# Optimization experiments

Hardware: AMD Instinct MI355X
Metric: run time of the kernel (lower is better)

The kernel has to match this reference:

```python
import jax, jax.numpy as jnp
import numpy as np

B, L, DIN, DH, DE = 16, 128, 768, 300, 100
ALPHA = 0.2
NEG = -9e15


def setup_inputs() -> dict:
    key = jax.random.key(0)
    k = jax.random.split(key, 7)
    s = lambda fan: 1.0 / np.sqrt(fan)
    return {
        "x": jax.random.normal(k[0], (B, L, DIN), jnp.float32),
        "adj": jax.random.randint(k[1], (B, L, L), 0, 2, jnp.int32),
        "edge_embedding": jax.random.normal(k[2], (B, L, L, DE), jnp.float32),
        "W": jax.random.normal(k[3], (DIN, DH), jnp.float32) * s(DIN),
        "a": jax.random.normal(k[4], (2 * DH, 1), jnp.float32) * s(2 * DH),
        "edge_map_w": jax.random.normal(k[5], (DH, DE), jnp.float32) * s(DE),
        "edge_map_b": jnp.zeros((DH,), jnp.float32),
        "edge_lin_w": jax.random.normal(k[6], (1, DH), jnp.float32) * s(DH),
        "edge_lin_b": jnp.zeros((1,), jnp.float32),
    }


def _forward(x, edge_embedding, W, a, edge_map_w, edge_map_b, edge_lin_w, edge_lin_b, adj):
    h = x @ W  # [B, L, DH]
    # Faithful to torch: h.repeat_interleave(L, dim=2).view(B, L*L, DH) scrambles
    # features: a_input_first[b, i*L+j, d] = h[b, i, (j*DH + d) // L].
    # So e1[b,i,j] = sum_d h[b,i,(j*DH+d)//L] * a[d] = h[b,i] . V[j], with V[j,k] =
    # sum of a[d] over d where (j*DH+d)//L == k. Build V once by scatter-add.
    idx = (jnp.arange(L)[:, None] * DH + jnp.arange(DH)[None, :]) // L  # [L, DH], values in [0, DH)
    a_first = a[:DH, 0]
    V = jnp.zeros((L, DH), h.dtype).at[jnp.arange(L)[:, None], idx].add(a_first[None, :])  # [L, DH]
    e1 = jnp.einsum('bik,jk->bij', h, V)  # [B, L, L]
    # Second half: h.repeat_interleave(L, dim=0).view(...) gives plain h_j tiling.
    e2 = h @ a[DH:, 0]  # [B, L], broadcast over i
    e = jax.nn.leaky_relu(e1 + e2[:, None, :], ALPHA)  # [B, L, L]
    # Edge-weight gate (use_edge_weight == 'yes'); note torch relu result is discarded.
    em = edge_embedding @ edge_map_w.T + edge_map_b  # [B, L, L, DH]
    ew = jax.nn.sigmoid(em @ edge_lin_w.T + edge_lin_b)[..., 0]  # [B, L, L]
    e_final = e * ew
    att = jax.nn.softmax(jnp.where(adj > 0, e_final, NEG), axis=2)  # dropout off (eval)
    return h + jnp.matmul(att, h)  # residual add, concat=False


def reference(x, adj, edge_embedding, W, a, edge_map_w, edge_map_b, edge_lin_w, edge_lin_b):
    return _forward(x, edge_embedding, W, a, edge_map_w, edge_map_b, edge_lin_w, edge_lin_b, adj)
```

## Files before the change

### kernel.cpp

```cpp
#include <hip/hip_runtime.h>
#include <hip/hip_bf16.h>


#define L 128
#define DH 300
#define DIN 768
#define DE 100
#define SPLITK 4
#define MROWS 2048
#define SL ((size_t)MROWS * DH)

typedef __bf16 bf16x8 __attribute__((ext_vector_type(8)));
typedef float f32x4 __attribute__((ext_vector_type(4)));
typedef unsigned short ushort_t;

__device__ __forceinline__ ushort_t f2bf(float f) {
    __bf16 h = (__bf16)f;
    ushort_t u;
    __builtin_memcpy(&u, &h, 2);
    return u;
}

__global__ __launch_bounds__(256) void k_small(
    const float* __restrict__ A,
    const float* __restrict__ EMW,
    const float* __restrict__ EMB,
    const float* __restrict__ ELW,
    const float* __restrict__ ELB,
    float* __restrict__ CV, float* __restrict__ C0,
    float* __restrict__ VW, int* __restrict__ VCOL)
{
    int t = threadIdx.x;
    if (blockIdx.x == 0) {
        if (t < DE) {
            float s = 0.f;
            for (int k = 0; k < DH; ++k)
                s += ELW[k] * EMW[k * DE + t];
            CV[t] = s;
        } else if (t == DE) {
            float s = 0.f;
            for (int k = 0; k < DH; ++k)
                s += ELW[k] * EMB[k];
            C0[0] = s + ELB[0];
        }
    } else {
        if (t < L) {
            int base = t * DH;
            int cm = base >> 7;
            float w0 = 0.f, w1 = 0.f, w2 = 0.f, w3 = 0.f;
            for (int j = 0; j < DH; ++j) {
                int u = ((base + j) >> 7) - cm;
                float av = A[j];
                w0 += (u == 0) ? av : 0.f;
                w1 += (u == 1) ? av : 0.f;
                w2 += (u == 2) ? av : 0.f;
                w3 += (u == 3) ? av : 0.f;
            }
            VCOL[t] = cm;
            VW[t * 4 + 0] = w0; VW[t * 4 + 1] = w1;
            VW[t * 4 + 2] = w2; VW[t * 4 + 3] = w3;
        }
    }
}

__global__ __launch_bounds__(256) void k_cvt(
    const float* __restrict__ Wm, ushort_t* __restrict__ WT)
{
    __shared__ float tile[64][65];
    int k0 = blockIdx.x * 64;
    int c0 = blockIdx.y * 64;
    int t = threadIdx.x;
#pragma unroll
    for (int s = 0; s < 16; ++s) {
        int idx = t + 256 * s;
        int kr = idx >> 6, cc = idx & 63;
        int c = c0 + cc;
        tile[kr][cc] = (c < DH) ? Wm[(size_t)(k0 + kr) * DH + c] : 0.f;
    }
    __syncthreads();
#pragma unroll
    for (int s = 0; s < 16; ++s) {
        int idx = t + 256 * s;
        int c = idx >> 6, kr = idx & 63;
        WT[(size_t)(c0 + c) * DIN + k0 + kr] = f2bf(tile[kr][c]);
    }
}

__global__ __launch_bounds__(256) void k_gemm(
    const float* __restrict__ X,
    const ushort_t* __restrict__ WT,
    float* __restrict__ HP)
{
    __shared__ ushort_t As[64 * 72];
    __shared__ ushort_t Bs[64 * 72];
    int t = threadIdx.x;
    int w = t >> 6;
    int lane = t & 63;
    int lr = lane & 15;
    int lk = lane >> 4;
    int r0 = blockIdx.y * 64;
    int c0 = blockIdx.x * 64;
    int kbase = blockIdx.z * (DIN / SPLITK);

    f32x4 acc[4];
#pragma unroll
    for (int ct = 0; ct < 4; ++ct) acc[ct] = (f32x4){0.f, 0.f, 0.f, 0.f};

    int srow = t >> 2, skq = (t & 3) * 16;

    for (int step = 0; step < 3; ++step) {
        int kk = kbase + step * 64;
        {
            const float4* xs = (const float4*)(X + (size_t)(r0 + srow) * DIN + kk + skq);
            float4 f0 = xs[0], f1 = xs[1], f2 = xs[2], f3 = xs[3];
            bf16x8 v0, v1;
            v0[0] = (__bf16)f0.x; v0[1] = (__bf16)f0.y; v0[2] = (__bf16)f0.z; v0[3] = (__bf16)f0.w;
            v0[4] = (__bf16)f1.x; v0[5] = (__bf16)f1.y; v0[6] = (__bf16)f1.z; v0[7] = (__bf16)f1.w;
            v1[0] = (__bf16)f2.x; v1[1] = (__bf16)f2.y; v1[2] = (__bf16)f2.z; v1[3] = (__bf16)f2.w;
            v1[4] = (__bf16)f3.x; v1[5] = (__bf16)f3.y; v1[6] = (__bf16)f3.z; v1[7] = (__bf16)f3.w;
            *(bf16x8*)&As[srow * 72 + skq] = v0;
            *(bf16x8*)&As[srow * 72 + skq + 8] = v1;
        }
        {
            const uint4* wp = (const uint4*)(WT + (size_t)(c0 + srow) * DIN + kk + skq);
            uint4 u0 = wp[0], u1 = wp[1];
            *(uint4*)&Bs[srow * 72 + skq] = u0;
            *(uint4*)&Bs[srow * 72 + skq + 8] = u1;
        }
        __syncthreads();
#pragma unroll
        for (int k2 = 0; k2 < 2; ++k2) {
            bf16x8 af = *(bf16x8*)&As[(w * 16 + lr) * 72 + k2 * 32 + lk * 8];
#pragma unroll
            for (int ct = 0; ct < 4; ++ct) {
                bf16x8 bf_ = *(bf16x8*)&Bs[(ct * 16 + lr) * 72 + k2 * 32 + lk * 8];
                acc[ct] = __builtin_amdgcn_mfma_f32_16x16x32_bf16(af, bf_, acc[ct], 0, 0, 0);
            }
        }
        __syncthreads();
    }
    float* outp = HP + (size_t)blockIdx.z * SL;
#pragma unroll
    for (int ct = 0; ct < 4; ++ct) {
        int col = c0 + ct * 16 + lr;
        if (col < DH) {
#pragma unroll
            for (int r = 0; r < 4; ++r) {
                int row = r0 + w * 16 + lk * 4 + r;
                outp[(size_t)row * DH + col] = acc[ct][r];
            }
        }
    }
}

__global__ __launch_bounds__(256) void k_red(
    const float* __restrict__ HP, const float* __restrict__ A,
    float* __restrict__ H, float* __restrict__ E2)
{
    int t = threadIdx.x;
    int row = blockIdx.x * 8 + (t >> 5);
    int lane = t & 31;
    const float4* a4 = (const float4*)(A + DH);
    float4* hout = (float4*)(H + (size_t)row * DH);
    float acc = 0.f;
    for (int k4 = lane; k4 < DH / 4; k4 += 32) {
        float4 hv; hv.x = 0.f; hv.y = 0.f; hv.z = 0.f; hv.w = 0.f;
#pragma unroll
        for (int z = 0; z < SPLITK; ++z) {
            float4 v = ((const float4*)(HP + (size_t)z * SL + (size_t)row * DH))[k4];
            hv.x += v.x; hv.y += v.y; hv.z += v.z; hv.w += v.w;
        }
        float4 av = a4[k4];
        hout[k4] = hv;
        acc += hv.x * av.x + hv.y * av.y + hv.z * av.z + hv.w * av.w;
    }
#pragma unroll
    for (int o = 16; o >= 1; o >>= 1) acc += __shfl_xor(acc, o);
    if (lane == 0) E2[row] = acc;
}

__global__ __launch_bounds__(256) void k_attn(
    const float* __restrict__ EE,
    const int* __restrict__ ADJ,
    const float* __restrict__ H,
    const float* __restrict__ E2,
    const float* __restrict__ CV, const float* __restrict__ C0,
    const float* __restrict__ VW, const int* __restrict__ VCOL,
    float* __restrict__ OUT)
{
    __shared__ float hrow[DH];
    __shared__ float cl[DE];
    __shared__ float ef[L];
    __shared__ float att[L];
    __shared__ float red[4];

    int bid = blockIdx.x;
    int b = bid >> 7;
    int t = threadIdx.x;

    for (int k = t; k < DH; k += 256) hrow[k] = H[(size_t)bid * DH + k];
    if (t < DE) cl[t] = CV[t];
    __syncthreads();

    {
        int j = t >> 1, half = t & 1;
        const float2* p = (const float2*)(EE + (size_t)bid * (L * DE) + j * DE + half * 50);
        const float* cp = cl + half * 50;
        float s = 0.f;
#pragma unroll
        for (int q = 0; q < 25; ++q) {
            float2 v = p[q];
            s = fmaf(v.x, cp[2 * q], s);
            s = fmaf(v.y, cp[2 * q + 1], s);
        }
        s += __shfl_xor(s, 1);
        float ewv = 1.f / (1.f + expf(-(s + C0[0])));

        int cm = VCOL[j];
        float e1 = 0.f;
#pragma unroll
        for (int u = 0; u < 4; ++u) {
            int c = cm + u; if (c > DH - 1) c = DH - 1;
            e1 += VW[j * 4 + u] * hrow[c];
        }
        float e = e1 + E2[(size_t)b * L + j];
        e = (e > 0.f) ? e : 0.2f * e;
        float efv = (ADJ[(size_t)bid * L + j] > 0) ? e * ewv : -9.0e15f;
        if (half == 0) ef[j] = efv;
    }
    __syncthreads();

    float v = (t < L) ? ef[t] : -3.0e38f;
#pragma unroll
    for (int o = 32; o >= 1; o >>= 1) v = fmaxf(v, __shfl_xor(v, o));
    int wid = t >> 6;
    if ((t & 63) == 0) red[wid] = v;
    __syncthreads();
    float mx = fmaxf(fmaxf(red[0], red[1]), fmaxf(red[2], red[3]));
    __syncthreads();
    float p = (t < L) ? expf(ef[t] - mx) : 0.f;
    v = p;
#pragma unroll
    for (int o = 32; o >= 1; o >>= 1) v += __shfl_xor(v, o);
    if ((t & 63) == 0) red[wid] = v;
    __syncthreads();
    float denom = red[0] + red[1] + red[2] + red[3];
    if (t < L) att[t] = p / denom;
    __syncthreads();

    const float* Hb = H + (size_t)b * L * DH;
    for (int k = t; k < DH; k += 256) {
        float a0 = hrow[k], a1 = 0.f, a2 = 0.f, a3 = 0.f;
#pragma unroll 4
        for (int j = 0; j < L; j += 4) {
            a0 = fmaf(att[j + 0], Hb[(size_t)(j + 0) * DH + k], a0);
            a1 = fmaf(att[j + 1], Hb[(size_t)(j + 1) * DH + k], a1);
            a2 = fmaf(att[j + 2], Hb[(size_t)(j + 2) * DH + k], a2);
            a3 = fmaf(att[j + 3], Hb[(size_t)(j + 3) * DH + k], a3);
        }
        OUT[(size_t)bid * DH + k] = (a0 + a1) + (a2 + a3);
    }
}

extern "C" void kernel_launch(void* const* d_in, const int* in_sizes, int n_in,
                              void* d_out, int out_size, void* d_ws, size_t ws_size,
                              hipStream_t stream) {
    const float* X   = (const float*)d_in[0];
    const int*   ADJ = (const int*)d_in[1];
    const float* EE  = (const float*)d_in[2];
    const float* Wm  = (const float*)d_in[3];
    const float* A   = (const float*)d_in[4];
    const float* EMW = (const float*)d_in[5];
    const float* EMB = (const float*)d_in[6];
    const float* ELW = (const float*)d_in[7];
    const float* ELB = (const float*)d_in[8];
    float* OUT = (float*)d_out;

    float* ws = (float*)d_ws;
    float* HP   = ws;
    float* H    = ws + 2457600;
    float* E2   = ws + 3072000;
    float* CV   = ws + 3074048;
    float* C0   = ws + 3074148;
    float* VW   = ws + 3074152;
    int*   VCOL = (int*)(ws + 3074664);
    ushort_t* WT = (ushort_t*)(ws + 3074816);

    k_small<<<dim3(2), dim3(256), 0, stream>>>(A, EMW, EMB, ELW, ELB, CV, C0, VW, VCOL);
    k_cvt<<<dim3(12, 5), dim3(256), 0, stream>>>(Wm, WT);
    k_gemm<<<dim3(5, 32, SPLITK), dim3(256), 0, stream>>>(X, WT, HP);
    k_red<<<dim3(256), dim3(256), 0, stream>>>(HP, A, H, E2);
    k_attn<<<dim3(2048), dim3(256), 0, stream>>>(EE, ADJ, H, E2, CV, C0, VW, VCOL, OUT);
}
```

Measured before the change: 72.68 us.

## Fuse W conversion and split-K reduction into GEMM, restructure edge-gate loads

Drops the separate W transpose/convert kernel and the split-K partial-sum reduction kernel. The GEMM now reads fp32 W directly, converts and transposes it into shared memory, runs the full K loop, and writes H plus E2 through shuffle reductions and atomicAdd. The pre-kernel zeroes E2 and computes the small vectors with parallel partial sums. The attention kernel loads each block's edge-embedding tile with coalesced 16-byte loads and reduces through shared memory. This removes two launches and the partial-sum round trip, at the cost of only 160 GEMM blocks, uncoalesced scalar shared stores for B, and atomics.

```diff
diff --git a/kernel.cpp b/kernel.cpp
--- a/kernel.cpp
+++ b/kernel.cpp
@@ -6,90 +6,69 @@
 #define DH 300
 #define DIN 768
 #define DE 100
-#define SPLITK 4
 #define MROWS 2048
-#define SL ((size_t)MROWS * DH)
 
 typedef __bf16 bf16x8 __attribute__((ext_vector_type(8)));
 typedef float f32x4 __attribute__((ext_vector_type(4)));
 typedef unsigned short ushort_t;
 
-__device__ __forceinline__ ushort_t f2bf(float f) {
-    __bf16 h = (__bf16)f;
-    ushort_t u;
-    __builtin_memcpy(&u, &h, 2);
-    return u;
-}
-
-__global__ __launch_bounds__(256) void k_small(
-    const float* __restrict__ A,
-    const float* __restrict__ EMW,
-    const float* __restrict__ EMB,
-    const float* __restrict__ ELW,
+__global__ __launch_bounds__(256) void k_pre(
+    const float* __restrict__ A, const float* __restrict__ EMW,
+    const float* __restrict__ EMB, const float* __restrict__ ELW,
     const float* __restrict__ ELB,
     float* __restrict__ CV, float* __restrict__ C0,
-    float* __restrict__ VW, int* __restrict__ VCOL)
+    float* __restrict__ VW, int* __restrict__ VCOL,
+    float* __restrict__ E2)
 {
+    __shared__ float Als[304];
     int t = threadIdx.x;
     if (blockIdx.x == 0) {
-        if (t < DE) {
+        float part = 0.f;
+        int d = t >> 1, g = t & 1;
+        if (d < DE) {
+            int k0 = g * 150;
+            for (int k = k0; k < k0 + 150; ++k)
+                part = fmaf(ELW[k], EMW[k * DE + d], part);
+        }
+        part += __shfl_xor(part, 1);
+        if (d < DE && g == 0) CV[d] = part;
+        if (t < 64) {
             float s = 0.f;
-            for (int k = 0; k < DH; ++k)
-                s += ELW[k] * EMW[k * DE + t];
-            CV[t] = s;
-        } else if (t == DE) {
-            float s = 0.f;
-            for (int k = 0; k < DH; ++k)
-                s += ELW[k] * EMB[k];
-            C0[0] = s + ELB[0];
+            for (int k = t; k < DH; k += 64) s = fmaf(ELW[k], EMB[k], s);
+#pragma unroll
+            for (int o = 32; o >= 1; o >>= 1) s += __shfl_xor(s, o);
+            if (t == 0) C0[0] = s + ELB[0];
         }
     } else {
+        for (int idx = t; idx < MROWS; idx += 256) E2[idx] = 0.f;
+        for (int idx = t; idx < DH; idx += 256) Als[idx] = A[idx];
+        __syncthreads();
         if (t < L) {
             int base = t * DH;
             int cm = base >> 7;
-            float w0 = 0.f, w1 = 0.f, w2 = 0.f, w3 = 0.f;
-            for (int j = 0; j < DH; ++j) {
-                int u = ((base + j) >> 7) - cm;
-                float av = A[j];
-                w0 += (u == 0) ? av : 0.f;
-                w1 += (u == 1) ? av : 0.f;
-                w2 += (u == 2) ? av : 0.f;
-                w3 += (u == 3) ? av : 0.f;
+            float w[4];
+#pragma unroll
+            for (int u = 0; u < 4; ++u) {
+                int js = 128 * (cm + u) - base;
+                int je = js + 128;
+                if (js < 0) js = 0;
+                if (je > DH) je = DH;
+                float s = 0.f;
+                for (int j = js; j < je; ++j) s += Als[j];
+                w[u] = (je > js) ? s : 0.f;
             }
             VCOL[t] = cm;
-            VW[t * 4 + 0] = w0; VW[t * 4 + 1] = w1;
-            VW[t * 4 + 2] = w2; VW[t * 4 + 3] = w3;
-        }
-    }
-}
-
-__global__ __launch_bounds__(256) void k_cvt(
-    const float* __restrict__ Wm, ushort_t* __restrict__ WT)
-{
-    __shared__ float tile[64][65];
-    int k0 = blockIdx.x * 64;
-    int c0 = blockIdx.y * 64;
-    int t = threadIdx.x;
-#pragma unroll
-    for (int s = 0; s < 16; ++s) {
-        int idx = t + 256 * s;
-        int kr = idx >> 6, cc = idx & 63;
-        int c = c0 + cc;
-        tile[kr][cc] = (c < DH) ? Wm[(size_t)(k0 + kr) * DH + c] : 0.f;
-    }
-    __syncthreads();
-#pragma unroll
-    for (int s = 0; s < 16; ++s) {
-        int idx = t + 256 * s;
-        int c = idx >> 6, kr = idx & 63;
-        WT[(size_t)(c0 + c) * DIN + k0 + kr] = f2bf(tile[kr][c]);
+            VW[t * 4 + 0] = w[0]; VW[t * 4 + 1] = w[1];
+            VW[t * 4 + 2] = w[2]; VW[t * 4 + 3] = w[3];
+        }
     }
 }
 
 __global__ __launch_bounds__(256) void k_gemm(
     const float* __restrict__ X,
-    const ushort_t* __restrict__ WT,
-    float* __restrict__ HP)
+    const float* __restrict__ Wm,
+    const float* __restrict__ A,
+    float* __restrict__ H, float* __restrict__ E2)
 {
     __shared__ ushort_t As[64 * 72];
     __shared__ ushort_t Bs[64 * 72];
@@ -100,16 +79,16 @@
     int lk = lane >> 4;
     int r0 = blockIdx.y * 64;
     int c0 = blockIdx.x * 64;
-    int kbase = blockIdx.z * (DIN / SPLITK);
 
     f32x4 acc[4];
 #pragma unroll
     for (int ct = 0; ct < 4; ++ct) acc[ct] = (f32x4){0.f, 0.f, 0.f, 0.f};
 
     int srow = t >> 2, skq = (t & 3) * 16;
-
-    for (int step = 0; step < 3; ++step) {
-        int kk = kbase + step * 64;
+    int bc4 = t & 15, bkr = t >> 4;
+
+    for (int step = 0; step < 12; ++step) {
+        int kk = step * 64;
         {
             const float4* xs = (const float4*)(X + (size_t)(r0 + srow) * DIN + kk + skq);
             float4 f0 = xs[0], f1 = xs[1], f2 = xs[2], f3 = xs[3];
@@ -121,11 +100,17 @@
             *(bf16x8*)&As[srow * 72 + skq] = v0;
             *(bf16x8*)&As[srow * 72 + skq + 8] = v1;
         }
-        {
-            const uint4* wp = (const uint4*)(WT + (size_t)(c0 + srow) * DIN + kk + skq);
-            uint4 u0 = wp[0], u1 = wp[1];
-            *(uint4*)&Bs[srow * 72 + skq] = u0;
-            *(uint4*)&Bs[srow * 72 + skq + 8] = u1;
+#pragma unroll
+        for (int p = 0; p < 4; ++p) {
+            int krow = bkr + p * 16;
+            int col = c0 + bc4 * 4;
+            float4 v;
+            if (col + 3 < DH) v = *(const float4*)(Wm + (size_t)(kk + krow) * DH + col);
+            else { v.x = 0.f; v.y = 0.f; v.z = 0.f; v.w = 0.f; }
+            Bs[(bc4 * 4 + 0) * 72 + krow] = (ushort_t)__builtin_bit_cast(unsigned short, (__bf16)v.x);
+            Bs[(bc4 * 4 + 1) * 72 + krow] = (ushort_t)__builtin_bit_cast(unsigned short, (__bf16)v.y);
+            Bs[(bc4 * 4 + 2) * 72 + krow] = (ushort_t)__builtin_bit_cast(unsigned short, (__bf16)v.z);
+            Bs[(bc4 * 4 + 3) * 72 + krow] = (ushort_t)__builtin_bit_cast(unsigned short, (__bf16)v.w);
         }
         __syncthreads();
 #pragma unroll
@@ -139,44 +124,28 @@
         }
         __syncthreads();
     }
-    float* outp = HP + (size_t)blockIdx.z * SL;
+    float a2v[4];
 #pragma unroll
     for (int ct = 0; ct < 4; ++ct) {
-        int col = c0 + ct * 16 + lr;
-        if (col < DH) {
-#pragma unroll
-            for (int r = 0; r < 4; ++r) {
-                int row = r0 + w * 16 + lk * 4 + r;
-                outp[(size_t)row * DH + col] = acc[ct][r];
-            }
-        }
-    }
-}
-
-__global__ __launch_bounds__(256) void k_red(
-    const float* __restrict__ HP, const float* __restrict__ A,
-    float* __restrict__ H, float* __restrict__ E2)
-{
-    int t = threadIdx.x;
-    int row = blockIdx.x * 8 + (t >> 5);
-    int lane = t & 31;
-    const float4* a4 = (const float4*)(A + DH);
-    float4* hout = (float4*)(H + (size_t)row * DH);
-    float acc = 0.f;
-    for (int k4 = lane; k4 < DH / 4; k4 += 32) {
-        float4 hv; hv.x = 0.f; hv.y = 0.f; hv.z = 0.f; hv.w = 0.f;
-#pragma unroll
-        for (int z = 0; z < SPLITK; ++z) {
-            float4 v = ((const float4*)(HP + (size_t)z * SL + (size_t)row * DH))[k4];
-            hv.x += v.x; hv.y += v.y; hv.z += v.z; hv.w += v.w;
-        }
-        float4 av = a4[k4];
-        hout[k4] = hv;
-        acc += hv.x * av.x + hv.y * av.y + hv.z * av.z + hv.w * av.w;
-    }
-#pragma unroll
-    for (int o = 16; o >= 1; o >>= 1) acc += __shfl_xor(acc, o);
-    if (lane == 0) E2[row] = acc;
+        int col = ct * 16 + lr;
+        a2v[ct] = (c0 + col < DH) ? A[DH + c0 + col] : 0.f;
+    }
+#pragma unroll
+    for (int r = 0; r < 4; ++r) {
+        int row = r0 + w * 16 + lk * 4 + r;
+        float e2p = 0.f;
+#pragma unroll
+        for (int ct = 0; ct < 4; ++ct) {
+            int col = c0 + ct * 16 + lr;
+            if (col < DH) H[(size_t)row * DH + col] = acc[ct][r];
+            e2p = fmaf(acc[ct][r], a2v[ct], e2p);
+        }
+        e2p += __shfl_xor(e2p, 1);
+        e2p += __shfl_xor(e2p, 2);
+        e2p += __shfl_xor(e2p, 4);
+        e2p += __shfl_xor(e2p, 8);
+        if (lr == 0) atomicAdd(&E2[row], e2p);
+    }
 }
 
 __global__ __launch_bounds__(256) void k_attn(
@@ -188,8 +157,9 @@
     const float* __restrict__ VW, const int* __restrict__ VCOL,
     float* __restrict__ OUT)
 {
+    __shared__ __align__(16) float cl[DE];
+    __shared__ float ps[3200];
     __shared__ float hrow[DH];
-    __shared__ float cl[DE];
     __shared__ float ef[L];
     __shared__ float att[L];
     __shared__ float red[4];
@@ -197,55 +167,71 @@
     int bid = blockIdx.x;
     int b = bid >> 7;
     int t = threadIdx.x;
+    const f32x4* src = (const f32x4*)(EE + (size_t)bid * (L * DE));
+
+    f32x4 v[13];
+#pragma unroll
+    for (int s = 0; s < 12; ++s) v[s] = src[t + 256 * s];
+    if (t < 128) v[12] = src[t + 3072];
+    else { v[12][0] = 0.f; v[12][1] = 0.f; v[12][2] = 0.f; v[12][3] = 0.f; }
 
     for (int k = t; k < DH; k += 256) hrow[k] = H[(size_t)bid * DH + k];
     if (t < DE) cl[t] = CV[t];
     __syncthreads();
 
+    int p = t % 25;
+#pragma unroll
+    for (int s = 0; s < 13; ++s) {
+        int idx = t + 256 * s;
+        if (s < 12 || t < 128) {
+            const float4 c4 = *(const float4*)&cl[p * 4];
+            ps[idx] = v[s][0] * c4.x + v[s][1] * c4.y + v[s][2] * c4.z + v[s][3] * c4.w;
+        }
+        p += 6; if (p >= 25) p -= 25;
+    }
+    __syncthreads();
+
     {
-        int j = t >> 1, half = t & 1;
-        const float2* p = (const float2*)(EE + (size_t)bid * (L * DE) + j * DE + half * 50);
-        const float* cp = cl + half * 50;
-        float s = 0.f;
-#pragma unroll
-        for (int q = 0; q < 25; ++q) {
-            float2 v = p[q];
-            s = fmaf(v.x, cp[2 * q], s);
-            s = fmaf(v.y, cp[2 * q + 1], s);
-        }
-        s += __shfl_xor(s, 1);
-        float ewv = 1.f / (1.f + expf(-(s + C0[0])));
-
-        int cm = VCOL[j];
-        float e1 = 0.f;
-#pragma unroll
-        for (int u = 0; u < 4; ++u) {
-            int c = cm + u; if (c > DH - 1) c = DH - 1;
-            e1 += VW[j * 4 + u] * hrow[c];
-        }
-        float e = e1 + E2[(size_t)b * L + j];
-        e = (e > 0.f) ? e : 0.2f * e;
-        float efv = (ADJ[(size_t)bid * L + j] > 0) ? e * ewv : -9.0e15f;
-        if (half == 0) ef[j] = efv;
-    }
-    __syncthreads();
-
-    float v = (t < L) ? ef[t] : -3.0e38f;
-#pragma unroll
-    for (int o = 32; o >= 1; o >>= 1) v = fmaxf(v, __shfl_xor(v, o));
+        int r = t >> 1, h = t & 1;
+        const float* pp = ps + 25 * r + h * 13;
+        float s0 = 0.f;
+#pragma unroll
+        for (int m = 0; m < 12; ++m) s0 += pp[m];
+        if (h == 0) s0 += pp[12];
+        s0 += __shfl_xor(s0, 1);
+        if (h == 0) {
+            float sv = s0 + C0[0];
+            float ewv = 1.f / (1.f + expf(-sv));
+            int cm = VCOL[r];
+            float e1 = 0.f;
+#pragma unroll
+            for (int u = 0; u < 4; ++u) {
+                int c = cm + u; if (c > DH - 1) c = DH - 1;
+                e1 += VW[r * 4 + u] * hrow[c];
+            }
+            float e = e1 + E2[(size_t)b * L + r];
+            e = (e > 0.f) ? e : 0.2f * e;
+            ef[r] = (ADJ[(size_t)bid * L + r] > 0) ? e * ewv : -9.0e15f;
+        }
+    }
+    __syncthreads();
+
+    float vv = (t < L) ? ef[t] : -3.0e38f;
+#pragma unroll
+    for (int o = 32; o >= 1; o >>= 1) vv = fmaxf(vv, __shfl_xor(vv, o));
     int wid = t >> 6;
-    if ((t & 63) == 0) red[wid] = v;
+    if ((t & 63) == 0) red[wid] = vv;
     __syncthreads();
     float mx = fmaxf(fmaxf(red[0], red[1]), fmaxf(red[2], red[3]));
     __syncthreads();
-    float p = (t < L) ? expf(ef[t] - mx) : 0.f;
-    v = p;
-#pragma unroll
-    for (int o = 32; o >= 1; o >>= 1) v += __shfl_xor(v, o);
-    if ((t & 63) == 0) red[wid] = v;
+    float pe = (t < L) ? expf(ef[t] - mx) : 0.f;
+    vv = pe;
+#pragma unroll
+    for (int o = 32; o >= 1; o >>= 1) vv += __shfl_xor(vv, o);
+    if ((t & 63) == 0) red[wid] = vv;
     __syncthreads();
     float denom = red[0] + red[1] + red[2] + red[3];
-    if (t < L) att[t] = p / denom;
+    if (t < L) att[t] = pe / denom;
     __syncthreads();
 
     const float* Hb = H + (size_t)b * L * DH;
@@ -277,18 +263,14 @@
     float* OUT = (float*)d_out;
 
     float* ws = (float*)d_ws;
-    float* HP   = ws;
-    float* H    = ws + 2457600;
-    float* E2   = ws + 3072000;
-    float* CV   = ws + 3074048;
-    float* C0   = ws + 3074148;
-    float* VW   = ws + 3074152;
-    int*   VCOL = (int*)(ws + 3074664);
-    ushort_t* WT = (ushort_t*)(ws + 3074816);
-
-    k_small<<<dim3(2), dim3(256), 0, stream>>>(A, EMW, EMB, ELW, ELB, CV, C0, VW, VCOL);
-    k_cvt<<<dim3(12, 5), dim3(256), 0, stream>>>(Wm, WT);
-    k_gemm<<<dim3(5, 32, SPLITK), dim3(256), 0, stream>>>(X, WT, HP);
-    k_red<<<dim3(256), dim3(256), 0, stream>>>(HP, A, H, E2);
+    float* H    = ws;
+    float* E2   = ws + 614400;
+    float* CV   = ws + 616448;
+    float* C0   = ws + 616548;
+    float* VW   = ws + 616552;
+    int*   VCOL = (int*)(ws + 617064);
+
+    k_pre<<<dim3(2), dim3(256), 0, stream>>>(A, EMW, EMB, ELW, ELB, CV, C0, VW, VCOL, E2);
+    k_gemm<<<dim3(5, 32), dim3(256), 0, stream>>>(X, Wm, A, H, E2);
     k_attn<<<dim3(2048), dim3(256), 0, stream>>>(EE, ADJ, H, E2, CV, C0, VW, VCOL, OUT);
 }
```

Result: no change. 72.17 us (-0.7%).
